# Performance work log

Measured on AMD Instinct MI355X. Metric: run time of the kernel, lower is better.

Reference implementation:

```python
import jax, jax.numpy as jnp
import numpy as np

HEIGHT = 256
WIDTH = 256
SIGMAINV = 7000.0  # DIB-R style soft-silhouette sharpness
EPS = 1e-10


def setup_inputs():
    key = jax.random.key(0)
    k1, k2, k3, k4, k5 = jax.random.split(key, 5)
    B, P, F = 1, 160, 256
    TH = TW = 1024
    points_bxpx3 = 0.8 * jax.random.normal(k1, (B, P, 3), jnp.float32)
    faces_fx3 = jax.random.randint(k2, (F, 3), 0, P)
    camera_rot_bx3x3 = jnp.broadcast_to(jnp.eye(3, dtype=jnp.float32), (B, 3, 3))
    camera_pos_bx3 = jnp.tile(jnp.array([[0.0, 0.0, 2.5]], jnp.float32), (B, 1))
    camera_proj_3x1 = jnp.array([[2.5], [2.5], [-1.0]], jnp.float32)
    uv_bxpx2 = jax.random.uniform(k3, (B, P, 2), jnp.float32)
    ft_fx3 = jax.random.randint(k4, (F, 3), 0, P)
    texture_bx3xthxtw = jax.random.uniform(k5, (B, 3, TH, TW), jnp.float32)
    return {"points_bxpx3": points_bxpx3, "faces_fx3": faces_fx3,
            "camera_rot_bx3x3": camera_rot_bx3x3, "camera_pos_bx3": camera_pos_bx3,
            "camera_proj_3x1": camera_proj_3x1, "uv_bxpx2": uv_bxpx2,
            "ft_fx3": ft_fx3, "texture_bx3xthxtw": texture_bx3xthxtw}


def _perspective(points_bxpx3, faces_fx3, cam_rot, cam_pos, cam_proj):
    p = points_bxpx3 - cam_pos[:, None, :]
    p = jnp.einsum('bpj,bij->bpi', p, cam_rot)                  # camera frame [B,P,3]
    xy3 = p * cam_proj.reshape(1, 1, 3)
    xy = xy3[..., :2] / xy3[..., 2:3]                           # projected 2D [B,P,2]
    pf0 = p[:, faces_fx3[:, 0]]
    pf1 = p[:, faces_fx3[:, 1]]
    pf2 = p[:, faces_fx3[:, 2]]
    points3d_bxfx9 = jnp.concatenate([pf0, pf1, pf2], axis=2)
    points2d_bxfx6 = jnp.concatenate([xy[:, faces_fx3[:, 0]], xy[:, faces_fx3[:, 1]], xy[:, faces_fx3[:, 2]]], axis=2)
    normal_bxfx3 = jnp.cross(pf1 - pf0, pf2 - pf0)
    return points3d_bxfx9, points2d_bxfx6, normal_bxfx3


def _edge_dist2(px, py, ax, ay, bx, by):
    ex, ey = bx - ax, by - ay
    t = jnp.clip(((px - ax) * ex + (py - ay) * ey) / (ex * ex + ey * ey + EPS), 0.0, 1.0)
    dx, dy = px - (ax + t * ex), py - (ay + t * ey)
    return dx * dx + dy * dy


def _rasterize(points3d_bxfx9, points2d_bxfx6, normalz_bxfx1, feat_bxfx9, H, W):
    B, F, _ = points2d_bxfx6.shape
    x0, y0, x1, y1, x2, y2 = [points2d_bxfx6[:, None, :, i] for i in range(6)]   # [B,1,F]
    xs = (jnp.arange(W, dtype=jnp.float32) + 0.5) / W * 2.0 - 1.0
    ys = 1.0 - (jnp.arange(H, dtype=jnp.float32) + 0.5) / H * 2.0
    px = jnp.tile(xs[None, :], (H, 1)).reshape(1, -1, 1)                          # [1,N,1]
    py = jnp.tile(ys[:, None], (1, W)).reshape(1, -1, 1)
    A = (x1 - x0) * (y2 - y0) - (x2 - x0) * (y1 - y0)
    invA = jnp.where(jnp.abs(A) > EPS, 1.0 / jnp.where(jnp.abs(A) > EPS, A, 1.0), 0.0)
    w0 = ((x1 - px) * (y2 - py) - (x2 - px) * (y1 - py)) * invA                   # [B,N,F]
    w1 = ((x2 - px) * (y0 - py) - (x0 - px) * (y2 - py)) * invA
    w2 = 1.0 - w0 - w1
    valid = (jnp.abs(A) > EPS) & (normalz_bxfx1[:, None, :, 0] > 0)               # backface cull
    inside = (w0 >= 0) & (w1 >= 0) & (w2 >= 0) & valid
    z0 = points3d_bxfx9[:, None, :, 2]
    z1 = points3d_bxfx9[:, None, :, 5]
    z2 = points3d_bxfx9[:, None, :, 8]
    z = w0 * z0 + w1 * z1 + w2 * z2                                               # camera looks down -z
    fid = jnp.argmax(jnp.where(inside, z, -1e10), axis=2)                          # nearest covering face
    hit = jnp.any(inside, axis=2)
    take = lambda a: jnp.take_along_axis(a, fid[:, :, None], axis=2)[:, :, 0]
    w0s, w1s, w2s = take(w0), take(w1), take(w2)
    fverts = feat_bxfx9.reshape(B, F, 3, 3)
    fsel = jax.vmap(lambda fv, ii: fv[ii])(fverts, fid)                            # [B,N,3verts,3feat]
    imfeat = (w0s[..., None] * fsel[:, :, 0] + w1s[..., None] * fsel[:, :, 1] + w2s[..., None] * fsel[:, :, 2])
    imfeat = imfeat * hit[..., None].astype(imfeat.dtype)
    # soft silhouette probability (DIB-R): 1 - prod_f (1 - exp(-d^2 * sigmainv))
    d2 = jnp.minimum(_edge_dist2(px, py, x0, y0, x1, y1),
                     jnp.minimum(_edge_dist2(px, py, x1, y1, x2, y2),
                                 _edge_dist2(px, py, x2, y2, x0, y0)))
    d2 = jnp.where(inside, 0.0, d2)
    log_miss = jnp.log(jnp.clip(1.0 - jnp.exp(-d2 * SIGMAINV), 1e-10, 1.0))
    improb = 1.0 - jnp.exp(jnp.sum(jnp.where(valid, log_miss, 0.0), axis=2))
    return imfeat.reshape(B, H, W, 3), improb.reshape(B, H, W, 1)


def _fragmentshader(imtexcoord_bxhxwx2, texture_bx3xthxtw, hardmask_bxhxwx1):
    th, tw = texture_bx3xthxtw.shape[2], texture_bx3xthxtw.shape[3]
    x = imtexcoord_bxhxwx2[..., 0] * (tw - 1)
    y = (1.0 - imtexcoord_bxhxwx2[..., 1]) * (th - 1)
    x0f = jnp.clip(jnp.floor(x), 0, tw - 1)
    y0f = jnp.clip(jnp.floor(y), 0, th - 1)
    x0 = x0f.astype(jnp.int32)
    y0 = y0f.astype(jnp.int32)
    x1 = jnp.clip(x0 + 1, 0, tw - 1)
    y1 = jnp.clip(y0 + 1, 0, th - 1)
    wx = jnp.clip(x - x0f, 0.0, 1.0)[..., None]
    wy = jnp.clip(y - y0f, 0.0, 1.0)[..., None]
    tex = texture_bx3xthxtw.transpose(0, 2, 3, 1)                                 # [B,th,tw,3]
    g = jax.vmap(lambda t, yy, xx: t[yy, xx])
    c00, c01 = g(tex, y0, x0), g(tex, y0, x1)
    c10, c11 = g(tex, y1, x0), g(tex, y1, x1)
    color = (c00 * (1 - wx) + c01 * wx) * (1 - wy) + (c10 * (1 - wx) + c11 * wx) * wy
    return jnp.clip(color * hardmask_bxhxwx1, 0.0, 1.0)


def reference(points_bxpx3, faces_fx3, camera_rot_bx3x3, camera_pos_bx3, camera_proj_3x1, uv_bxpx2, ft_fx3, texture_bx3xthxtw):
    points3d, points2d, normal = _perspective(points_bxpx3, faces_fx3, camera_rot_bx3x3, camera_pos_bx3, camera_proj_3x1)
    normalz = normal[:, :, 2:3]
    normal1 = normal / (jnp.sqrt(jnp.sum(normal * normal, axis=2, keepdims=True)) + EPS)
    c0 = uv_bxpx2[:, ft_fx3[:, 0]]
    c1 = uv_bxpx2[:, ft_fx3[:, 1]]
    c2 = uv_bxpx2[:, ft_fx3[:, 2]]
    mask = jnp.ones_like(c0[:, :, :1])
    uv_bxfx9 = jnp.concatenate([c0, mask, c1, mask, c2, mask], axis=2)
    imfeat, improb = _rasterize(points3d, points2d, normalz, uv_bxfx9, HEIGHT, WIDTH)
    imrender = _fragmentshader(imfeat[..., :2], texture_bx3xthxtw, imfeat[..., 2:3])
    return imrender, improb, normal1
```

## Files before the change

kernel.cpp:

```cpp
#include <hip/hip_runtime.h>
#include <math.h>

#define HGT 256
#define WID 256
#define NF 256
#define NP 160
#define SIGMAINV 7000.0f
#define EPSF 1e-10f
#define TW 1024
#define TH 1024
#define CHUNKS 8
#define FPC 32
#define PPB 64
#define NTHR 512
#define CUT2 3.29e-3f

__device__ __forceinline__ float mul_opaque(float a, float b)
{
    float r;
    asm volatile("v_mul_f32 %0, %1, %2" : "=v"(r) : "v"(a), "v"(b));
    return r;
}
__device__ __forceinline__ float fma_opaque(float a, float b, float c)
{
    float r;
    asm volatile("v_fma_f32 %0, %1, %2, %3" : "=v"(r) : "v"(a), "v"(b), "v"(c));
    return r;
}

__global__ __launch_bounds__(NTHR) void render_fused(
    const float* __restrict__ pts,
    const int*   __restrict__ faces,
    const float* __restrict__ rot,
    const float* __restrict__ cpos,
    const float* __restrict__ proj,
    const float* __restrict__ uvs,
    const int*   __restrict__ ft,
    const float* __restrict__ tex,
    float*       __restrict__ out)
{
    __shared__ float4 sgeo4[NF * 5];
    __shared__ float  scratch[NTHR * 3];

    float* sp  = scratch;
    float* sxy = scratch + 480;
    float* sZ   = scratch;
    float* sLog = scratch + NTHR;
    int*   sFid = (int*)(scratch + 2 * NTHR);

    const int t = threadIdx.x;

    const float r00 = rot[0], r01 = rot[1], r02 = rot[2];
    const float r10 = rot[3], r11 = rot[4], r12 = rot[5];
    const float r20 = rot[6], r21 = rot[7], r22 = rot[8];
    const float cx = cpos[0], cy = cpos[1], cz = cpos[2];
    const float p0 = proj[0], p1 = proj[1], p2 = proj[2];

    if (t < NP) {
        float ax = pts[t * 3 + 0] - cx;
        float ay = pts[t * 3 + 1] - cy;
        float az = pts[t * 3 + 2] - cz;
        float qx = r00 * ax + r01 * ay + r02 * az;
        float qy = r10 * ax + r11 * ay + r12 * az;
        float qz = r20 * ax + r21 * ay + r22 * az;
        sp[t * 3 + 0] = qx; sp[t * 3 + 1] = qy; sp[t * 3 + 2] = qz;
        float zz = qz * p2;
        sxy[t * 2 + 0] = (qx * p0) / zz;
        sxy[t * 2 + 1] = (qy * p1) / zz;
    }
    __syncthreads();

    if (t < NF) {
        int i0 = faces[t * 3 + 0], i1 = faces[t * 3 + 1], i2 = faces[t * 3 + 2];
        float ax = sp[i0 * 3 + 0], ay = sp[i0 * 3 + 1], az = sp[i0 * 3 + 2];
        float bx = sp[i1 * 3 + 0], by = sp[i1 * 3 + 1], bz = sp[i1 * 3 + 2];
        float gx = sp[i2 * 3 + 0], gy = sp[i2 * 3 + 1], gz = sp[i2 * 3 + 2];

        float e1x = bx - ax, e1y = by - ay, e1z = bz - az;
        float e2x = gx - ax, e2y = gy - ay, e2z = gz - az;
        float tnx = mul_opaque(e1z, e2y);
        float nx  = fma_opaque(e1y, e2z, -tnx);
        float tny = mul_opaque(e1x, e2z);
        float ny  = fma_opaque(e1z, e2x, -tny);
        float tnz = mul_opaque(e1y, e2x);
        float nz  = fma_opaque(e1x, e2y, -tnz);
        if (blockIdx.x == 0) {
            float s  = (mul_opaque(nx, nx) + mul_opaque(ny, ny)) + mul_opaque(nz, nz);
            float nl = sqrtf(s) + 1e-10f;
            float* out_normal = out + HGT * WID * 3 + HGT * WID;
            out_normal[t * 3 + 0] = nx / nl;
            out_normal[t * 3 + 1] = ny / nl;
            out_normal[t * 3 + 2] = nz / nl;
        }

        float x0 = sxy[i0 * 2 + 0], y0 = sxy[i0 * 2 + 1];
        float x1 = sxy[i1 * 2 + 0], y1 = sxy[i1 * 2 + 1];
        float x2 = sxy[i2 * 2 + 0], y2 = sxy[i2 * 2 + 1];
        float A = mul_opaque(x1 - x0, y2 - y0) - mul_opaque(x2 - x0, y1 - y0);
        bool okA = fabsf(A) > EPSF;
        bool valid = okA && (nz > 0.0f);
        float invA = okA ? 1.0f / A : 0.0f;

        float4 q0;
        if (valid) {
            q0.x = fminf(fminf(x0, x1), x2);
            q0.y = fminf(fminf(y0, y1), y2);
            q0.z = fmaxf(fmaxf(x0, x1), x2);
            q0.w = fmaxf(fmaxf(y0, y1), y2);
        } else {
            q0.x = 1e30f; q0.y = 1e30f; q0.z = -1e30f; q0.w = -1e30f;
        }
        float e0xp = x1 - x0, e0yp = y1 - y0;
        float e1xp = x2 - x1, e1yp = y2 - y1;
        float e2xp = x0 - x2, e2yp = y0 - y2;
        float iee0 = 1.0f / (e0xp * e0xp + e0yp * e0yp + EPSF);
        float iee1 = 1.0f / (e1xp * e1xp + e1yp * e1yp + EPSF);
        float iee2 = 1.0f / (e2xp * e2xp + e2yp * e2yp + EPSF);

        sgeo4[t * 5 + 0] = q0;
        sgeo4[t * 5 + 1] = make_float4(x0, y0, x1, y1);
        sgeo4[t * 5 + 2] = make_float4(x2, y2, invA, az);
        sgeo4[t * 5 + 3] = make_float4(bz, gz, 0.0f, 0.0f);
        sgeo4[t * 5 + 4] = make_float4(iee0, iee1, iee2, 0.0f);
    }
    __syncthreads();

    const int chunk = t >> 6;
    const int p     = t & 63;
    const int tx = (blockIdx.x & 31) * 8;
    const int ty = (blockIdx.x >> 5) * 8;
    {
        const int w = tx + (p & 7);
        const int h = ty + (p >> 3);
        const float px = ((float)w + 0.5f) / (float)WID * 2.0f - 1.0f;
        const float py = 1.0f - ((float)h + 0.5f) / (float)HGT * 2.0f;

        float best_z = -1e30f;
        int   fid = 0;
        float logsum = 0.0f;

        const int f0 = chunk * FPC;
        for (int f = f0; f < f0 + FPC; ++f) {
            float4 q0 = sgeo4[f * 5 + 0];
            float ddx = fmaxf(fmaxf(q0.x - px, px - q0.z), 0.0f);
            float ddy = fmaxf(fmaxf(q0.y - py, py - q0.w), 0.0f);
            if (ddx * ddx + ddy * ddy > CUT2) continue;

            float4 q1 = sgeo4[f * 5 + 1];
            float4 q2 = sgeo4[f * 5 + 2];

            float ax = q1.z - px, ay = q1.w - py;
            float bx = q2.x - px, by = q2.y - py;
            float gx = q1.x - px, gy = q1.y - py;
            float w0 = (ax * by - bx * ay) * q2.z;
            float w1 = (bx * gy - gx * by) * q2.z;
            float w2 = 1.0f - w0 - w1;
            bool inside = (w0 >= 0.0f) & (w1 >= 0.0f) & (w2 >= 0.0f);
            if (inside) {
                float4 q3 = sgeo4[f * 5 + 3];
                float z = w0 * q2.w + w1 * q3.x + w2 * q3.y;
                if (z > best_z) { best_z = z; fid = f; }
                logsum += -23.025850929940457f;
            } else {
                float4 q4 = sgeo4[f * 5 + 4];
                bool s0 = (w0 < 0.0f);
                bool s1 = (w1 < 0.0f);
                float Sx  = s0 ? ax   : (s1 ? bx   : gx);
                float Sy  = s0 ? ay   : (s1 ? by   : gy);
                float Tx  = s0 ? bx   : (s1 ? gx   : ax);
                float Ty  = s0 ? by   : (s1 ? gy   : ay);
                float iee = s0 ? q4.y : (s1 ? q4.z : q4.x);
                float Ex = Tx - Sx, Ey = Ty - Sy;
                float tt = fminf(fmaxf(-(Sx * Ex + Sy * Ey) * iee, 0.0f), 1.0f);
                float dx = fmaf(tt, Ex, Sx), dy = fmaf(tt, Ey, Sy);
                float d2 = dx * dx + dy * dy;

                float a = d2 * SIGMAINV;
                if (a < 23.03f) {
                    float e = __expf(-a);
                    logsum += __logf(fmaxf(1.0f - e, 1e-10f));
                }
            }
        }
        sZ[t] = best_z; sFid[t] = fid; sLog[t] = logsum;
    }
    __syncthreads();

    if (t < PPB) {
        float bz = -1e30f; int bf = 0; float ls = 0.0f;
        #pragma unroll
        for (int c = 0; c < CHUNKS; ++c) {
            int i = c * PPB + t;
            ls += sLog[i];
            float z = sZ[i];
            if (z > bz) { bz = z; bf = sFid[i]; }
        }
        bool hit = bz > -1e29f;

        const int w = tx + (t & 7);
        const int h = ty + (t >> 3);
        const int pix = h * WID + w;
        out[HGT * WID * 3 + pix] = 1.0f - __expf(ls);

        float cr = 0.0f, cg = 0.0f, cb = 0.0f;
        if (hit) {
            const float px = ((float)w + 0.5f) / (float)WID * 2.0f - 1.0f;
            const float py = 1.0f - ((float)h + 0.5f) / (float)HGT * 2.0f;
            float4 q1 = sgeo4[bf * 5 + 1];
            float4 q2 = sgeo4[bf * 5 + 2];
            float axx = q1.z - px, ayy = q1.w - py;
            float bxx = q2.x - px, byy = q2.y - py;
            float gxx = q1.x - px, gyy = q1.y - py;
            float w0 = (axx * byy - bxx * ayy) * q2.z;
            float w1 = (bxx * gyy - gxx * byy) * q2.z;
            float w2 = 1.0f - w0 - w1;
            int j0 = ft[bf * 3 + 0], j1 = ft[bf * 3 + 1], j2 = ft[bf * 3 + 2];
            float u = w0 * uvs[j0 * 2 + 0] + w1 * uvs[j1 * 2 + 0] + w2 * uvs[j2 * 2 + 0];
            float v = w0 * uvs[j0 * 2 + 1] + w1 * uvs[j1 * 2 + 1] + w2 * uvs[j2 * 2 + 1];
            float mask = w0 + w1 + w2;

            float x = u * (float)(TW - 1);
            float y = (1.0f - v) * (float)(TH - 1);
            float x0f = fminf(fmaxf(floorf(x), 0.0f), (float)(TW - 1));
            float y0f = fminf(fmaxf(floorf(y), 0.0f), (float)(TH - 1));
            int xi0 = (int)x0f, yi0 = (int)y0f;
            int xi1 = min(xi0 + 1, TW - 1);
            int yi1 = min(yi0 + 1, TH - 1);
            float wx = fminf(fmaxf(x - x0f, 0.0f), 1.0f);
            float wy = fminf(fmaxf(y - y0f, 0.0f), 1.0f);

            int o00 = yi0 * TW + xi0, o01 = yi0 * TW + xi1;
            int o10 = yi1 * TW + xi0, o11 = yi1 * TW + xi1;
            #pragma unroll
            for (int c = 0; c < 3; ++c) {
                const float* tp = tex + c * (TW * TH);
                float c00 = tp[o00], c01 = tp[o01], c10 = tp[o10], c11 = tp[o11];
                float col = (c00 * (1.0f - wx) + c01 * wx) * (1.0f - wy)
                          + (c10 * (1.0f - wx) + c11 * wx) * wy;
                col = fminf(fmaxf(col * mask, 0.0f), 1.0f);
                if (c == 0) cr = col; else if (c == 1) cg = col; else cb = col;
            }
        }
        out[pix * 3 + 0] = cr;
        out[pix * 3 + 1] = cg;
        out[pix * 3 + 2] = cb;
    }
}

extern "C" void kernel_launch(void* const* d_in, const int* in_sizes, int n_in,
                              void* d_out, int out_size, void* d_ws, size_t ws_size,
                              hipStream_t stream)
{
    const float* pts   = (const float*)d_in[0];
    const int*   faces = (const int*)  d_in[1];
    const float* rot   = (const float*)d_in[2];
    const float* cpos  = (const float*)d_in[3];
    const float* proj  = (const float*)d_in[4];
    const float* uvs   = (const float*)d_in[5];
    const int*   ft    = (const int*)  d_in[6];
    const float* tex   = (const float*)d_in[7];
    float* out = (float*)d_out;

    render_fused<<<(HGT * WID) / PPB, NTHR, 0, stream>>>(
        pts, faces, rot, cpos, proj, uvs, ft, tex, out);
}
```

Before: 88.75 us.

## Process two pixels per thread with wave-shuffle reduction and branchless soft-coverage product

Each block now covers 128 pixels: every thread handles two vertically adjacent pixels against one 32-face chunk. The eight chunks of a pixel sit in neighbouring lanes and are combined with xor shuffles, replacing the shared-memory reduction and the second barrier. The per-face log-sum of coverage becomes a running product of (1-exp) factors computed branchlessly for both inside and outside cases, which removes the per-face log and divergent branches. This halves the grid and reuses the bounding-box test across two pixels, at the cost of more registers, always computing the edge-distance path, and possible underflow differences from multiplying probabilities directly.

```diff
diff --git a/kernel.cpp b/kernel.cpp
--- a/kernel.cpp
+++ b/kernel.cpp
@@ -11,7 +11,7 @@
 #define TH 1024
 #define CHUNKS 8
 #define FPC 32
-#define PPB 64
+#define PPB 128
 #define NTHR 512
 #define CUT2 3.29e-3f
 
@@ -40,13 +40,10 @@
     float*       __restrict__ out)
 {
     __shared__ float4 sgeo4[NF * 5];
-    __shared__ float  scratch[NTHR * 3];
+    __shared__ float  scratch[800];
 
     float* sp  = scratch;
     float* sxy = scratch + 480;
-    float* sZ   = scratch;
-    float* sLog = scratch + NTHR;
-    int*   sFid = (int*)(scratch + 2 * NTHR);
 
     const int t = threadIdx.x;
 
@@ -125,30 +122,39 @@
     }
     __syncthreads();
 
-    const int chunk = t >> 6;
-    const int p     = t & 63;
-    const int tx = (blockIdx.x & 31) * 8;
-    const int ty = (blockIdx.x >> 5) * 8;
-    {
-        const int w = tx + (p & 7);
-        const int h = ty + (p >> 3);
-        const float px = ((float)w + 0.5f) / (float)WID * 2.0f - 1.0f;
-        const float py = 1.0f - ((float)h + 0.5f) / (float)HGT * 2.0f;
-
-        float best_z = -1e30f;
-        int   fid = 0;
-        float logsum = 0.0f;
-
-        const int f0 = chunk * FPC;
-        for (int f = f0; f < f0 + FPC; ++f) {
-            float4 q0 = sgeo4[f * 5 + 0];
-            float ddx = fmaxf(fmaxf(q0.x - px, px - q0.z), 0.0f);
-            float ddy = fmaxf(fmaxf(q0.y - py, py - q0.w), 0.0f);
-            if (ddx * ddx + ddy * ddy > CUT2) continue;
-
-            float4 q1 = sgeo4[f * 5 + 1];
-            float4 q2 = sgeo4[f * 5 + 2];
-
+    const int s = t >> 3;
+    const int c = t & 7;
+    const int tx = (blockIdx.x & 15) * 16;
+    const int ty = (blockIdx.x >> 4) * 8;
+    const int w  = tx + (s & 15);
+    const int h0 = ty + 2 * (s >> 4);
+    const int h1 = h0 + 1;
+    const float px  = ((float)w + 0.5f) / (float)WID * 2.0f - 1.0f;
+    const float py0 = 1.0f - ((float)h0 + 0.5f) / (float)HGT * 2.0f;
+    const float py1 = 1.0f - ((float)h1 + 0.5f) / (float)HGT * 2.0f;
+
+    float bz0 = -1e30f, bz1 = -1e30f;
+    int   bf0 = 0,      bf1 = 0;
+    float pr0 = 1.0f,   pr1 = 1.0f;
+
+    const int f0 = c * FPC;
+    for (int f = f0; f < f0 + FPC; ++f) {
+        float4 q0 = sgeo4[f * 5 + 0];
+        float ddx  = fmaxf(fmaxf(q0.x - px, px - q0.z), 0.0f);
+        float ddy0 = fmaxf(fmaxf(q0.y - py0, py0 - q0.w), 0.0f);
+        float ddy1 = fmaxf(fmaxf(q0.y - py1, py1 - q0.w), 0.0f);
+        float bd0 = ddx * ddx + ddy0 * ddy0;
+        float bd1 = ddx * ddx + ddy1 * ddy1;
+        if (fminf(bd0, bd1) > CUT2) continue;
+
+        float4 q1 = sgeo4[f * 5 + 1];
+        float4 q2 = sgeo4[f * 5 + 2];
+        float4 q3 = sgeo4[f * 5 + 3];
+        float4 q4 = sgeo4[f * 5 + 4];
+
+        #pragma unroll
+        for (int k = 0; k < 2; ++k) {
+            float py = k ? py1 : py0;
             float ax = q1.z - px, ay = q1.w - py;
             float bx = q2.x - px, by = q2.y - py;
             float gx = q1.x - px, gy = q1.y - py;
@@ -156,94 +162,98 @@
             float w1 = (bx * gy - gx * by) * q2.z;
             float w2 = 1.0f - w0 - w1;
             bool inside = (w0 >= 0.0f) & (w1 >= 0.0f) & (w2 >= 0.0f);
-            if (inside) {
-                float4 q3 = sgeo4[f * 5 + 3];
-                float z = w0 * q2.w + w1 * q3.x + w2 * q3.y;
-                if (z > best_z) { best_z = z; fid = f; }
-                logsum += -23.025850929940457f;
+            float z = w0 * q2.w + w1 * q3.x + w2 * q3.y;
+
+            bool s0 = (w0 < 0.0f);
+            bool s1 = (w1 < 0.0f);
+            float Sx  = s0 ? ax   : (s1 ? bx   : gx);
+            float Sy  = s0 ? ay   : (s1 ? by   : gy);
+            float Tx  = s0 ? bx   : (s1 ? gx   : ax);
+            float Ty  = s0 ? by   : (s1 ? gy   : ay);
+            float iee = s0 ? q4.y : (s1 ? q4.z : q4.x);
+            float Ex = Tx - Sx, Ey = Ty - Sy;
+            float tt = fminf(fmaxf(-(Sx * Ex + Sy * Ey) * iee, 0.0f), 1.0f);
+            float dx = fmaf(tt, Ex, Sx), dy = fmaf(tt, Ey, Sy);
+            float d2 = dx * dx + dy * dy;
+            float a = d2 * SIGMAINV;
+            float fct = fmaxf(1.0f - __expf(-a), 1e-10f);
+            fct = (a < 23.03f) ? fct : 1.0f;
+            fct = inside ? 1e-10f : fct;
+
+            if (k == 0) {
+                if (inside && z > bz0) { bz0 = z; bf0 = f; }
+                pr0 *= fct;
             } else {
-                float4 q4 = sgeo4[f * 5 + 4];
-                bool s0 = (w0 < 0.0f);
-                bool s1 = (w1 < 0.0f);
-                float Sx  = s0 ? ax   : (s1 ? bx   : gx);
-                float Sy  = s0 ? ay   : (s1 ? by   : gy);
-                float Tx  = s0 ? bx   : (s1 ? gx   : ax);
-                float Ty  = s0 ? by   : (s1 ? gy   : ay);
-                float iee = s0 ? q4.y : (s1 ? q4.z : q4.x);
-                float Ex = Tx - Sx, Ey = Ty - Sy;
-                float tt = fminf(fmaxf(-(Sx * Ex + Sy * Ey) * iee, 0.0f), 1.0f);
-                float dx = fmaf(tt, Ex, Sx), dy = fmaf(tt, Ey, Sy);
-                float d2 = dx * dx + dy * dy;
-
-                float a = d2 * SIGMAINV;
-                if (a < 23.03f) {
-                    float e = __expf(-a);
-                    logsum += __logf(fmaxf(1.0f - e, 1e-10f));
+                if (inside && z > bz1) { bz1 = z; bf1 = f; }
+                pr1 *= fct;
+            }
+        }
+    }
+
+    #pragma unroll
+    for (int m = 1; m <= 4; m <<= 1) {
+        float oz0 = __shfl_xor(bz0, m); int of0 = __shfl_xor(bf0, m);
+        float op0 = __shfl_xor(pr0, m);
+        float oz1 = __shfl_xor(bz1, m); int of1 = __shfl_xor(bf1, m);
+        float op1 = __shfl_xor(pr1, m);
+        if (oz0 > bz0 || (oz0 == bz0 && of0 < bf0)) { bz0 = oz0; bf0 = of0; }
+        if (oz1 > bz1 || (oz1 == bz1 && of1 < bf1)) { bz1 = oz1; bf1 = of1; }
+        pr0 *= op0;
+        pr1 *= op1;
+    }
+
+    if (c == 0) {
+        #pragma unroll
+        for (int k = 0; k < 2; ++k) {
+            int   h   = k ? h1  : h0;
+            float py  = k ? py1 : py0;
+            float bz  = k ? bz1 : bz0;
+            int   bf  = k ? bf1 : bf0;
+            float pr  = k ? pr1 : pr0;
+            const int pix = h * WID + w;
+            out[HGT * WID * 3 + pix] = 1.0f - pr;
+
+            float cr = 0.0f, cg = 0.0f, cb = 0.0f;
+            if (bz > -1e29f) {
+                float4 q1 = sgeo4[bf * 5 + 1];
+                float4 q2 = sgeo4[bf * 5 + 2];
+                float axx = q1.z - px, ayy = q1.w - py;
+                float bxx = q2.x - px, byy = q2.y - py;
+                float gxx = q1.x - px, gyy = q1.y - py;
+                float w0 = (axx * byy - bxx * ayy) * q2.z;
+                float w1 = (bxx * gyy - gxx * byy) * q2.z;
+                float w2 = 1.0f - w0 - w1;
+                int j0 = ft[bf * 3 + 0], j1 = ft[bf * 3 + 1], j2 = ft[bf * 3 + 2];
+                float u = w0 * uvs[j0 * 2 + 0] + w1 * uvs[j1 * 2 + 0] + w2 * uvs[j2 * 2 + 0];
+                float v = w0 * uvs[j0 * 2 + 1] + w1 * uvs[j1 * 2 + 1] + w2 * uvs[j2 * 2 + 1];
+                float mask = w0 + w1 + w2;
+
+                float x = u * (float)(TW - 1);
+                float y = (1.0f - v) * (float)(TH - 1);
+                float x0f = fminf(fmaxf(floorf(x), 0.0f), (float)(TW - 1));
+                float y0f = fminf(fmaxf(floorf(y), 0.0f), (float)(TH - 1));
+                int xi0 = (int)x0f, yi0 = (int)y0f;
+                int xi1 = min(xi0 + 1, TW - 1);
+                int yi1 = min(yi0 + 1, TH - 1);
+                float wx = fminf(fmaxf(x - x0f, 0.0f), 1.0f);
+                float wy = fminf(fmaxf(y - y0f, 0.0f), 1.0f);
+
+                int o00 = yi0 * TW + xi0, o01 = yi0 * TW + xi1;
+                int o10 = yi1 * TW + xi0, o11 = yi1 * TW + xi1;
+                #pragma unroll
+                for (int ch = 0; ch < 3; ++ch) {
+                    const float* tp = tex + ch * (TW * TH);
+                    float c00 = tp[o00], c01 = tp[o01], c10 = tp[o10], c11 = tp[o11];
+                    float col = (c00 * (1.0f - wx) + c01 * wx) * (1.0f - wy)
+                              + (c10 * (1.0f - wx) + c11 * wx) * wy;
+                    col = fminf(fmaxf(col * mask, 0.0f), 1.0f);
+                    if (ch == 0) cr = col; else if (ch == 1) cg = col; else cb = col;
                 }
             }
-        }
-        sZ[t] = best_z; sFid[t] = fid; sLog[t] = logsum;
-    }
-    __syncthreads();
-
-    if (t < PPB) {
-        float bz = -1e30f; int bf = 0; float ls = 0.0f;
-        #pragma unroll
-        for (int c = 0; c < CHUNKS; ++c) {
-            int i = c * PPB + t;
-            ls += sLog[i];
-            float z = sZ[i];
-            if (z > bz) { bz = z; bf = sFid[i]; }
-        }
-        bool hit = bz > -1e29f;
-
-        const int w = tx + (t & 7);
-        const int h = ty + (t >> 3);
-        const int pix = h * WID + w;
-        out[HGT * WID * 3 + pix] = 1.0f - __expf(ls);
-
-        float cr = 0.0f, cg = 0.0f, cb = 0.0f;
-        if (hit) {
-            const float px = ((float)w + 0.5f) / (float)WID * 2.0f - 1.0f;
-            const float py = 1.0f - ((float)h + 0.5f) / (float)HGT * 2.0f;
-            float4 q1 = sgeo4[bf * 5 + 1];
-            float4 q2 = sgeo4[bf * 5 + 2];
-            float axx = q1.z - px, ayy = q1.w - py;
-            float bxx = q2.x - px, byy = q2.y - py;
-            float gxx = q1.x - px, gyy = q1.y - py;
-            float w0 = (axx * byy - bxx * ayy) * q2.z;
-            float w1 = (bxx * gyy - gxx * byy) * q2.z;
-            float w2 = 1.0f - w0 - w1;
-            int j0 = ft[bf * 3 + 0], j1 = ft[bf * 3 + 1], j2 = ft[bf * 3 + 2];
-            float u = w0 * uvs[j0 * 2 + 0] + w1 * uvs[j1 * 2 + 0] + w2 * uvs[j2 * 2 + 0];
-            float v = w0 * uvs[j0 * 2 + 1] + w1 * uvs[j1 * 2 + 1] + w2 * uvs[j2 * 2 + 1];
-            float mask = w0 + w1 + w2;
-
-            float x = u * (float)(TW - 1);
-            float y = (1.0f - v) * (float)(TH - 1);
-            float x0f = fminf(fmaxf(floorf(x), 0.0f), (float)(TW - 1));
-            float y0f = fminf(fmaxf(floorf(y), 0.0f), (float)(TH - 1));
-            int xi0 = (int)x0f, yi0 = (int)y0f;
-            int xi1 = min(xi0 + 1, TW - 1);
-            int yi1 = min(yi0 + 1, TH - 1);
-            float wx = fminf(fmaxf(x - x0f, 0.0f), 1.0f);
-            float wy = fminf(fmaxf(y - y0f, 0.0f), 1.0f);
-
-            int o00 = yi0 * TW + xi0, o01 = yi0 * TW + xi1;
-            int o10 = yi1 * TW + xi0, o11 = yi1 * TW + xi1;
-            #pragma unroll
-            for (int c = 0; c < 3; ++c) {
-                const float* tp = tex + c * (TW * TH);
-                float c00 = tp[o00], c01 = tp[o01], c10 = tp[o10], c11 = tp[o11];
-                float col = (c00 * (1.0f - wx) + c01 * wx) * (1.0f - wy)
-                          + (c10 * (1.0f - wx) + c11 * wx) * wy;
-                col = fminf(fmaxf(col * mask, 0.0f), 1.0f);
-                if (c == 0) cr = col; else if (c == 1) cg = col; else cb = col;
-            }
-        }
-        out[pix * 3 + 0] = cr;
-        out[pix * 3 + 1] = cg;
-        out[pix * 3 + 2] = cb;
+            out[pix * 3 + 0] = cr;
+            out[pix * 3 + 1] = cg;
+            out[pix * 3 + 2] = cb;
+        }
     }
 }
 
```

Result: slower. 103.1 us (+16.2%).
